# Performance work log

Measured on AMD Instinct MI355X. Metric: run time of the kernel, lower is better.

## Reference

```python
import jax, jax.numpy as jnp
import numpy as np

B, S, F, E, C = 8, 8192, 512, 128, 1000


def setup_inputs() -> dict:
    key = jax.random.key(0)
    k1, k2, k3, k4 = jax.random.split(key, 4)
    x = jax.random.normal(k1, (B, F), dtype=jnp.float32)
    support_x = jax.random.normal(k2, (B, S, F), dtype=jnp.float32)
    support_y = jax.random.uniform(k3, (B, S, C), dtype=jnp.float32)
    # xavier_uniform on (1, F, E): gain * sqrt(6/(fan_in+fan_out))
    limit = float(np.sqrt(6.0 / (F + E)))
    proj_weight = jax.random.uniform(k4, (1, F, E), dtype=jnp.float32,
                                     minval=-limit, maxval=limit)
    return {"x": x, "support_x": support_x, "support_y": support_y,
            "proj_weight": proj_weight}


def reference(x, support_x, support_y, proj_weight):
    W = proj_weight[0]  # (F, E); bmm with repeated weight == shared matmul
    xq = x @ W                               # (B, E) query embedding
    sx = jnp.einsum('bsf,fe->bse', support_x, W)  # (B, S, E)
    # euclidean kernel: scores = -||xq - sx||_2, shape (B, S)
    diff = xq[:, None, :] - sx               # (B, S, E)
    scores = -jnp.sqrt(jnp.sum(diff * diff, axis=-1))
    probs = jax.nn.softmax(scores, axis=-1)  # (B, S)
    out = jnp.einsum('bs,bsc->bc', probs, support_y)  # (B, C)
    return out
```

## Files before the change

kernel.cpp:

```cpp
#include <hip/hip_runtime.h>
#include <hip/hip_bf16.h>

#define BB 8
#define SS 8192
#define FF 512
#define EE 128
#define CC 1000

typedef __bf16 bf16x8 __attribute__((ext_vector_type(8)));
typedef float  f32x4  __attribute__((ext_vector_type(4)));

__global__ void k0_wt(const float* __restrict__ W, __bf16* __restrict__ Wt) {
    int idx = blockIdx.x * 256 + threadIdx.x;
    int e = idx & (EE - 1);
    int f = idx >> 7;
    Wt[e * FF + f] = (__bf16)W[f * EE + e];
}

__global__ __launch_bounds__(256) void k1_scores(
    const float* __restrict__ x,
    const float* __restrict__ sx,
    const __bf16* __restrict__ Wt,
    float* __restrict__ scores)
{
    __shared__ __bf16 lA[2][4][128][8];
    __shared__ __bf16 lB[2][4][128][8];
    __shared__ float  scp[2][128];

    const int tid   = threadIdx.x;
    const int b     = blockIdx.x >> 6;
    const int srow0 = (blockIdx.x & 63) << 7;
    const float* Xb = sx + ((size_t)b * SS + srow0) * FF;
    const float* xb = x + b * FF;

    const int row  = tid >> 1;
    const int kh   = tid & 1;
    const int lane = tid & 63;
    const int w    = tid >> 6;
    const int wrow = (w >> 1) * 64;
    const int wcol = (w & 1) * 64;
    const int lg   = lane >> 4;
    const int lr   = lane & 15;

    f32x4 acc[4][4];
    #pragma unroll
    for (int m = 0; m < 4; m++)
        #pragma unroll
        for (int n = 0; n < 4; n++) { f32x4 z = {0.f, 0.f, 0.f, 0.f}; acc[m][n] = z; }

    float4 sReg[4], xReg[4];

    auto LOADT = [&](int t) {
        const float* pS = Xb + (size_t)row * FF + t * 32 + kh * 16;
        const float* pX = xb + t * 32 + kh * 16;
        #pragma unroll
        for (int i = 0; i < 4; i++) {
            sReg[i] = *(const float4*)(pS + 4 * i);
            xReg[i] = *(const float4*)(pX + 4 * i);
        }
    };
    auto WRITET = [&](int buf) {
        __bf16 d[16];
        #pragma unroll
        for (int i = 0; i < 4; i++) {
            d[4 * i + 0] = (__bf16)(xReg[i].x - sReg[i].x);
            d[4 * i + 1] = (__bf16)(xReg[i].y - sReg[i].y);
            d[4 * i + 2] = (__bf16)(xReg[i].z - sReg[i].z);
            d[4 * i + 3] = (__bf16)(xReg[i].w - sReg[i].w);
        }
        *(bf16x8*)&lA[buf][kh * 2 + 0][row][0] = *(bf16x8*)&d[0];
        *(bf16x8*)&lA[buf][kh * 2 + 1][row][0] = *(bf16x8*)&d[8];
    };
    auto STAGEB = [&](int buf, int t) {
        const __bf16* pW = Wt + (size_t)row * FF + t * 32 + kh * 16;
        bf16x8 w0 = *(const bf16x8*)(pW);
        bf16x8 w1 = *(const bf16x8*)(pW + 8);
        *(bf16x8*)&lB[buf][kh * 2 + 0][row][0] = w0;
        *(bf16x8*)&lB[buf][kh * 2 + 1][row][0] = w1;
    };

    LOADT(0);
    STAGEB(0, 0);
    WRITET(0);
    __syncthreads();

    for (int t = 0; t < 16; t++) {
        const int cur = t & 1;
        if (t < 15) {
            LOADT(t + 1);
            STAGEB(cur ^ 1, t + 1);
        }
        bf16x8 af[4], bfr[4];
        #pragma unroll
        for (int m = 0; m < 4; m++)
            af[m] = *(const bf16x8*)&lA[cur][lg][wrow + m * 16 + lr][0];
        #pragma unroll
        for (int n = 0; n < 4; n++)
            bfr[n] = *(const bf16x8*)&lB[cur][lg][wcol + n * 16 + lr][0];
        #pragma unroll
        for (int m = 0; m < 4; m++)
            #pragma unroll
            for (int n = 0; n < 4; n++)
                acc[m][n] = __builtin_amdgcn_mfma_f32_16x16x32_bf16(af[m], bfr[n], acc[m][n], 0, 0, 0);
        if (t < 15) WRITET(cur ^ 1);
        __syncthreads();
    }

    float rp[4][4];
    #pragma unroll
    for (int m = 0; m < 4; m++)
        #pragma unroll
        for (int j = 0; j < 4; j++) {
            float s = 0.f;
            #pragma unroll
            for (int n = 0; n < 4; n++) { float v = acc[m][n][j]; s += v * v; }
            rp[m][j] = s;
        }
    #pragma unroll
    for (int mask = 1; mask < 16; mask <<= 1)
        #pragma unroll
        for (int m = 0; m < 4; m++)
            #pragma unroll
            for (int j = 0; j < 4; j++)
                rp[m][j] += __shfl_xor(rp[m][j], mask);

    if (lr == 0) {
        #pragma unroll
        for (int m = 0; m < 4; m++)
            #pragma unroll
            for (int j = 0; j < 4; j++)
                scp[w & 1][wrow + m * 16 + lg * 4 + j] = rp[m][j];
    }
    __syncthreads();
    if (tid < 128) {
        float sum = scp[0][tid] + scp[1][tid];
        scores[(size_t)b * SS + srow0 + tid] = -sqrtf(sum);
    }
}

__global__ __launch_bounds__(256) void k3_wsum(
    const float* __restrict__ scores,
    const float* __restrict__ y,
    float* __restrict__ pout,
    float* __restrict__ pden)
{
    __shared__ float wv[64];
    const int b  = blockIdx.x >> 7;
    const int ch = blockIdx.x & 127;
    const int s0 = ch * 64;
    const int t  = threadIdx.x;

    if (t < 64) wv[t] = expf(scores[b * SS + s0 + t]);
    __syncthreads();

    if (t < 250) {
        float a0 = 0.f, a1 = 0.f, a2 = 0.f, a3 = 0.f;
        const float* base = y + ((size_t)b * SS + s0) * CC + t * 4;
        #pragma unroll 4
        for (int r = 0; r < 64; r++) {
            float4 v = *(const float4*)(base + (size_t)r * CC);
            float wgt = wv[r];
            a0 += wgt * v.x; a1 += wgt * v.y; a2 += wgt * v.z; a3 += wgt * v.w;
        }
        float4 res = {a0, a1, a2, a3};
        *(float4*)(pout + ((size_t)b * 128 + ch) * CC + t * 4) = res;
    }
    if (t == 0) {
        float d = 0.f;
        for (int r = 0; r < 64; r++) d += wv[r];
        pden[b * 128 + ch] = d;
    }
}

__global__ void k4_final(const float* __restrict__ pout, const float* __restrict__ pden,
                         float* __restrict__ out) {
    int idx = blockIdx.x * 256 + threadIdx.x;
    if (idx >= BB * CC) return;
    int b = idx / CC, c = idx % CC;
    float den = 0.f;
    for (int k = 0; k < 128; k++) den += pden[b * 128 + k];
    float num = 0.f;
    for (int k = 0; k < 128; k++) num += pout[((size_t)b * 128 + k) * CC + c];
    out[idx] = num / den;
}

extern "C" void kernel_launch(void* const* d_in, const int* in_sizes, int n_in,
                              void* d_out, int out_size, void* d_ws, size_t ws_size,
                              hipStream_t stream) {
    const float* x  = (const float*)d_in[0];
    const float* sx = (const float*)d_in[1];
    const float* sy = (const float*)d_in[2];
    const float* W  = (const float*)d_in[3];

    char* ws = (char*)d_ws;
    __bf16* Wt    = (__bf16*)(ws);
    float*  scores = (float*)(ws + 131072);
    float*  pout   = (float*)(ws + 131072 + 262144);
    float*  pden   = (float*)(ws + 131072 + 262144 + 4096000);

    k0_wt<<<256, 256, 0, stream>>>(W, Wt);
    k1_scores<<<512, 256, 0, stream>>>(x, sx, Wt, scores);
    k3_wsum<<<1024, 256, 0, stream>>>(scores, sy, pout, pden);
    k4_final<<<32, 256, 0, stream>>>(pout, pden, (float*)d_out);
}
```

Measured before the change: 100.7 us.

## Fuse score computation with weighted support-label sum in one kernel

Merges the score kernel and the weighted-sum kernel so each block computes distances for its 128 support rows, exponentiates them in shared memory, and immediately accumulates the weighted support_y rows. This removes the scores round-trip through global memory and one kernel launch, and halves the number of partials the final reduction reads. In exchange, the number of blocks streaming support_y drops from 1024 to 512, which may reduce memory-level parallelism on the largest read, and each block now does both the GEMM and the streaming phase serially.

```diff
diff --git a/kernel.cpp b/kernel.cpp
--- a/kernel.cpp
+++ b/kernel.cpp
@@ -17,19 +17,23 @@
     Wt[e * FF + f] = (__bf16)W[f * EE + e];
 }
 
-__global__ __launch_bounds__(256) void k1_scores(
+__global__ __launch_bounds__(256) void k_fused(
     const float* __restrict__ x,
     const float* __restrict__ sx,
     const __bf16* __restrict__ Wt,
-    float* __restrict__ scores)
+    const float* __restrict__ y,
+    float* __restrict__ pout,
+    float* __restrict__ pden)
 {
     __shared__ __bf16 lA[2][4][128][8];
     __shared__ __bf16 lB[2][4][128][8];
     __shared__ float  scp[2][128];
+    __shared__ float  wv[128];
 
     const int tid   = threadIdx.x;
     const int b     = blockIdx.x >> 6;
-    const int srow0 = (blockIdx.x & 63) << 7;
+    const int chunk = blockIdx.x & 63;
+    const int srow0 = chunk << 7;
     const float* Xb = sx + ((size_t)b * SS + srow0) * FF;
     const float* xb = x + b * FF;
 
@@ -132,43 +136,29 @@
                 scp[w & 1][wrow + m * 16 + lg * 4 + j] = rp[m][j];
     }
     __syncthreads();
-    if (tid < 128) {
-        float sum = scp[0][tid] + scp[1][tid];
-        scores[(size_t)b * SS + srow0 + tid] = -sqrtf(sum);
-    }
-}
-
-__global__ __launch_bounds__(256) void k3_wsum(
-    const float* __restrict__ scores,
-    const float* __restrict__ y,
-    float* __restrict__ pout,
-    float* __restrict__ pden)
-{
-    __shared__ float wv[64];
-    const int b  = blockIdx.x >> 7;
-    const int ch = blockIdx.x & 127;
-    const int s0 = ch * 64;
-    const int t  = threadIdx.x;
-
-    if (t < 64) wv[t] = expf(scores[b * SS + s0 + t]);
+    if (tid < 128)
+        wv[tid] = expf(-sqrtf(scp[0][tid] + scp[1][tid]));
     __syncthreads();
 
-    if (t < 250) {
+    if (w == 0) {
+        float d = wv[lane] + wv[lane + 64];
+        #pragma unroll
+        for (int mask = 1; mask < 64; mask <<= 1)
+            d += __shfl_xor(d, mask);
+        if (lane == 0) pden[b * 64 + chunk] = d;
+    }
+
+    if (tid < 250) {
         float a0 = 0.f, a1 = 0.f, a2 = 0.f, a3 = 0.f;
-        const float* base = y + ((size_t)b * SS + s0) * CC + t * 4;
+        const float* base = y + ((size_t)b * SS + srow0) * CC + tid * 4;
         #pragma unroll 4
-        for (int r = 0; r < 64; r++) {
+        for (int r = 0; r < 128; r++) {
             float4 v = *(const float4*)(base + (size_t)r * CC);
             float wgt = wv[r];
             a0 += wgt * v.x; a1 += wgt * v.y; a2 += wgt * v.z; a3 += wgt * v.w;
         }
         float4 res = {a0, a1, a2, a3};
-        *(float4*)(pout + ((size_t)b * 128 + ch) * CC + t * 4) = res;
-    }
-    if (t == 0) {
-        float d = 0.f;
-        for (int r = 0; r < 64; r++) d += wv[r];
-        pden[b * 128 + ch] = d;
+        *(float4*)(pout + ((size_t)(b * 64 + chunk)) * CC + tid * 4) = res;
     }
 }
 
@@ -178,9 +168,11 @@
     if (idx >= BB * CC) return;
     int b = idx / CC, c = idx % CC;
     float den = 0.f;
-    for (int k = 0; k < 128; k++) den += pden[b * 128 + k];
+    #pragma unroll 8
+    for (int k = 0; k < 64; k++) den += pden[b * 64 + k];
     float num = 0.f;
-    for (int k = 0; k < 128; k++) num += pout[((size_t)b * 128 + k) * CC + c];
+    #pragma unroll 8
+    for (int k = 0; k < 64; k++) num += pout[((size_t)(b * 64 + k)) * CC + c];
     out[idx] = num / den;
 }
 
@@ -193,13 +185,11 @@
     const float* W  = (const float*)d_in[3];
 
     char* ws = (char*)d_ws;
-    __bf16* Wt    = (__bf16*)(ws);
-    float*  scores = (float*)(ws + 131072);
-    float*  pout   = (float*)(ws + 131072 + 262144);
-    float*  pden   = (float*)(ws + 131072 + 262144 + 4096000);
+    __bf16* Wt   = (__bf16*)(ws);
+    float*  pout = (float*)(ws + 131072);
+    float*  pden = (float*)(ws + 131072 + 2048000);
 
     k0_wt<<<256, 256, 0, stream>>>(W, Wt);
-    k1_scores<<<512, 256, 0, stream>>>(x, sx, Wt, scores);
-    k3_wsum<<<1024, 256, 0, stream>>>(scores, sy, pout, pden);
+    k_fused<<<512, 256, 0, stream>>>(x, sx, Wt, sy, pout, pden);
     k4_final<<<32, 256, 0, stream>>>(pout, pden, (float*)d_out);
 }
```

Result: faster. 89.17 us (-11.4%).
